# Performance work log

Measured on AMD Instinct MI355X. Metric: run time of the kernel, lower is better.

Reference implementation:

```python
import jax, jax.numpy as jnp
import numpy as np

B, S, D, H = 4, 2048, 1024, 16
DK = D // H

def setup_inputs() -> dict:
    key = jax.random.key(0)
    ks = jax.random.split(key, 7)
    f = lambda k, shape: jax.random.normal(k, shape, dtype=jnp.float32)
    return {
        "query": f(ks[0], (B, S, D)),
        "key":   f(ks[1], (B, S, D)),
        "value": f(ks[2], (B, S, D)),
        "w_q": f(ks[3], (D, D)) * (D ** -0.5),
        "w_k": f(ks[4], (D, D)) * (D ** -0.5),
        "w_v": f(ks[5], (D, D)) * (D ** -0.5),
        "w_o": f(ks[6], (D, D)) * (D ** -0.5),
    }

def reference(query, key, value, w_q, w_k, w_v, w_o):
    # Linear layers: y = x @ W^T (torch nn.Linear convention), bias=False
    def split_heads(x):  # [B,S,D] -> [B,H,S,DK]
        return x.reshape(B, S, H, DK).transpose(0, 2, 1, 3)
    Q = split_heads(query @ w_q.T)
    K = split_heads(key @ w_k.T)
    V = split_heads(value @ w_v.T)
    scale = jnp.float32(1.0 / np.sqrt(DK))
    scores = jnp.einsum('bhqd,bhkd->bhqk', Q, K) * scale  # [B,H,Sq,Sk]
    attn = jax.nn.softmax(scores, axis=-1)
    out = jnp.einsum('bhqk,bhkd->bhqd', attn, V)  # [B,H,Sq,DK]
    out = out.transpose(0, 2, 1, 3).reshape(B, S, D)
    return out @ w_o.T
```

## Files before the change

### kernel.cpp

```cpp
#include <hip/hip_runtime.h>
#include <stdint.h>

#define NB 4
#define NS 2048
#define ND 1024
#define NH 16
#define NDK 64
#define NM (NB*NS)

typedef __attribute__((ext_vector_type(8))) short short8;
typedef __attribute__((ext_vector_type(8))) unsigned short ushort8v;
typedef __attribute__((ext_vector_type(4))) float f32x4;
typedef __attribute__((ext_vector_type(16))) float f32x16;

__device__ __forceinline__ unsigned short f2bf(float f) {
  union { float f; uint32_t u; } v; v.f = f;
  uint32_t u = v.u;
  return (unsigned short)((u + 0x7FFFu + ((u >> 16) & 1u)) >> 16);
}

__device__ __forceinline__ void gload16(const void* g, void* l) {
  __builtin_amdgcn_global_load_lds(
      (const __attribute__((address_space(1))) void*)g,
      (__attribute__((address_space(3))) void*)l, 16, 0, 0);
}

__device__ __forceinline__ int xcd_swz(int flat, int nwg) {
  return (flat & 7) * (nwg >> 3) + (flat >> 3);
}

__global__ void convert_all(
    const float* __restrict__ x0, const float* __restrict__ x1, const float* __restrict__ x2,
    const float* __restrict__ w0, const float* __restrict__ w1,
    const float* __restrict__ w2, const float* __restrict__ w3,
    unsigned short* __restrict__ ox0, unsigned short* __restrict__ ox1, unsigned short* __restrict__ ox2,
    unsigned short* __restrict__ ow0, unsigned short* __restrict__ ow1,
    unsigned short* __restrict__ ow2, unsigned short* __restrict__ ow3)
{
  const float* src;
  unsigned short* dst;
  size_t i;
  if (blockIdx.y < 3) {
    src = blockIdx.y == 0 ? x0 : (blockIdx.y == 1 ? x1 : x2);
    dst = blockIdx.y == 0 ? ox0 : (blockIdx.y == 1 ? ox1 : ox2);
    i = ((size_t)blockIdx.x * 256 + threadIdx.x) * 8;
  } else {
    if (blockIdx.x >= 2048) return;
    size_t e = ((size_t)blockIdx.x * 256 + threadIdx.x) * 8;
    int which = (int)(e >> 20);
    size_t off = e & ((1u << 20) - 1);
    const float* ws[4] = {w0, w1, w2, w3};
    unsigned short* wd[4] = {ow0, ow1, ow2, ow3};
    src = ws[which]; dst = wd[which]; i = off;
  }
  f32x4 a = *(const f32x4*)(src + i);
  f32x4 b = *(const f32x4*)(src + i + 4);
  ushort8v h;
  h[0]=f2bf(a.x); h[1]=f2bf(a.y); h[2]=f2bf(a.z); h[3]=f2bf(a.w);
  h[4]=f2bf(b.x); h[5]=f2bf(b.y); h[6]=f2bf(b.z); h[7]=f2bf(b.w);
  *(ushort8v*)(dst + i) = h;
}

template<int OUT, int PRESCALE, int BN>
__device__ __forceinline__ void gemm_bk32_core(
    const unsigned short* __restrict__ A,
    const unsigned short* __restrict__ Bt,
    void* __restrict__ Cout,
    unsigned short* lds, int m0, int n0)
{
  const int K = ND, N = ND;
  const int NBF = BN / 64;
  const int NBL = BN / 128;
  const int NL  = 2 + NBL;
  const int ASZ = 8192, BSZ = BN*32, SZ = ASZ + BSZ;
  const int NT = K / 32;
  const int tid = threadIdx.x;
  const int lane = tid & 63, wid = tid >> 6;
  const int l15 = lane & 15, lg = lane >> 4;
  const int wr = wid >> 2, wc = wid & 3;
  const float QSC = 0.125f * 1.44269504088896f;

  const unsigned short* Asrc[2];
  const unsigned short* Bsrc[2];
  int dofA[2], dofB[2];
#pragma unroll
  for (int l = 0; l < 2; ++l) {
    int cidx = l*512 + tid;
    int r = cidx >> 2;
    int ch = (cidx & 3) ^ ((r >> 1) & 3);
    Asrc[l] = A + (size_t)(m0 + r)*K + ch*8;
    dofA[l] = cidx * 8;
  }
#pragma unroll
  for (int l = 0; l < NBL; ++l) {
    int cidx = l*512 + tid;
    int r = cidx >> 2;
    int ch = (cidx & 3) ^ ((r >> 1) & 3);
    Bsrc[l] = Bt + (size_t)(n0 + r)*K + ch*8;
    dofB[l] = cidx * 8;
  }

  f32x4 acc[8][NBF] = {};

#define STAGE32(t, buf)                                                        \
  {                                                                            \
    unsigned short* d_ = lds + (buf)*SZ;                                       \
    _Pragma("unroll") for (int l = 0; l < 2; ++l)                              \
      gload16(Asrc[l] + (t)*32, d_ + dofA[l]);                                 \
    _Pragma("unroll") for (int l = 0; l < NBL; ++l)                            \
      gload16(Bsrc[l] + (t)*32, d_ + ASZ + dofB[l]);                           \
  }

  STAGE32(0, 0)
  STAGE32(1, 1)
  if (NBL == 2) asm volatile("s_waitcnt vmcnt(4)" ::: "memory");
  else          asm volatile("s_waitcnt vmcnt(3)" ::: "memory");
  __builtin_amdgcn_s_barrier();

  int b0 = 0;
  for (int t = 0; t < NT; ++t) {
    if (t + 2 < NT) {
      int nb = b0 + 2; if (nb >= 3) nb -= 3;
      STAGE32(t + 2, nb)
    }
    const unsigned short* Abase = lds + b0*SZ;
    const unsigned short* Bbase = lds + b0*SZ + ASZ;

    short8 bfr[NBF];
#pragma unroll
    for (int nn = 0; nn < NBF; ++nn) {
      int row = wc*(BN/4) + nn*16 + l15;
      bfr[nn] = *(const short8*)(Bbase + row*32 + (lg ^ ((row >> 1) & 3))*8);
    }
#pragma unroll
    for (int mh = 0; mh < 2; ++mh) {
      short8 af[4];
#pragma unroll
      for (int mm = 0; mm < 4; ++mm) {
        int row = wr*128 + mh*64 + mm*16 + l15;
        af[mm] = *(const short8*)(Abase + row*32 + (lg ^ ((row >> 1) & 3))*8);
      }
      __builtin_amdgcn_s_setprio(1);
#pragma unroll
      for (int mm = 0; mm < 4; ++mm)
#pragma unroll
        for (int nn = 0; nn < NBF; ++nn)
          acc[mh*4+mm][nn] = __builtin_amdgcn_mfma_f32_16x16x32_bf16(
              af[mm], bfr[nn], acc[mh*4+mm][nn], 0, 0, 0);
      __builtin_amdgcn_s_setprio(0);
    }

    if (t + 2 < NT) {
      if (NBL == 2) asm volatile("s_waitcnt vmcnt(4)" ::: "memory");
      else          asm volatile("s_waitcnt vmcnt(3)" ::: "memory");
      __builtin_amdgcn_s_barrier();
    } else if (t + 1 < NT) {
      asm volatile("s_waitcnt vmcnt(0)" ::: "memory");
      __builtin_amdgcn_s_barrier();
    }
    b0 = (b0 + 1 == 3) ? 0 : b0 + 1;
  }
#undef STAGE32

#pragma unroll
  for (int m = 0; m < 8; ++m)
#pragma unroll
    for (int n = 0; n < NBF; ++n)
#pragma unroll
      for (int i = 0; i < 4; ++i) {
        int row = m0 + wr*128 + m*16 + lg*4 + i;
        int col = n0 + wc*(BN/4) + n*16 + l15;
        float val = PRESCALE ? acc[m][n][i] * QSC : acc[m][n][i];
        if (OUT == 0)
          ((float*)Cout)[(size_t)row * N + col] = val;
        else if (OUT == 1)
          ((unsigned short*)Cout)[(size_t)row * N + col] = f2bf(val);
        else
          ((unsigned short*)Cout)[((size_t)((row >> 11)*1024 + col))*NS + (row & (NS-1))]
              = f2bf(val);
      }
}

__global__ __launch_bounds__(512, 1) void gemm_qkv(
    const unsigned short* __restrict__ Xq, const unsigned short* __restrict__ Wq, unsigned short* Qb,
    const unsigned short* __restrict__ Xk, const unsigned short* __restrict__ Wk, unsigned short* Kb,
    const unsigned short* __restrict__ Xv, const unsigned short* __restrict__ Wv, unsigned short* VbT)
{
  __shared__ unsigned short lds[3*16384];
  int flat = (blockIdx.z * 32 + blockIdx.y) * 4 + blockIdx.x;
  int swz = xcd_swz(flat, 384);
  int z = swz >> 7, rem = swz & 127;
  int m0 = (rem >> 2) * 256, n0 = (rem & 3) * 256;
  if (z == 0)      gemm_bk32_core<1,1,256>(Xq, Wq, Qb,  lds, m0, n0);
  else if (z == 1) gemm_bk32_core<1,0,256>(Xk, Wk, Kb,  lds, m0, n0);
  else             gemm_bk32_core<2,0,256>(Xv, Wv, VbT, lds, m0, n0);
}

__global__ __launch_bounds__(512, 1) void gemm_o(
    const unsigned short* __restrict__ A, const unsigned short* __restrict__ Bt, float* C)
{
  __shared__ unsigned short lds[3*12288];
  int flat = blockIdx.y * 8 + blockIdx.x;
  int swz = xcd_swz(flat, 256);
  gemm_bk32_core<0,0,128>(A, Bt, C, lds, (swz >> 3) * 256, (swz & 7) * 128);
}

__global__ __launch_bounds__(256, 2) void flash_attn(
    const unsigned short* __restrict__ Qb,
    const unsigned short* __restrict__ Kb,
    const unsigned short* __restrict__ VT,
    unsigned short* __restrict__ O)
{
  __shared__ unsigned short Kt[2][64*64];
  __shared__ unsigned short Vt[2][64*64];
  const int tid = threadIdx.x, lane = tid & 63, wid = tid >> 6;
  const int l31 = lane & 31, hi = lane >> 5;
  int flat = blockIdx.y * 8 + blockIdx.x;
  int swz = xcd_swz(flat, 512);
  const int bh = swz >> 3, b = bh >> 4, h = bh & 15;
  const int q0 = (swz & 7) * 256 + wid * 64;

  const unsigned short* Kp[2]; const unsigned short* Vp[2]; int dofs[2];
#pragma unroll
  for (int p = 0; p < 2; ++p) {
    int slot = tid + p*256;
    int g = slot >> 6, r = slot & 63;
    Kp[p] = Kb + ((size_t)(b*NS + r))*ND + h*64 + g*8;
    Vp[p] = VT + ((size_t)(bh*64 + r))*NS + g*8;
    dofs[p] = slot * 8;
  }

  short8 qf[2][4];
#pragma unroll
  for (int qs = 0; qs < 2; ++qs)
#pragma unroll
    for (int ks = 0; ks < 4; ++ks)
      qf[qs][ks] = *(const short8*)(Qb + (size_t)(b*NS + q0 + qs*32 + l31)*ND + h*64 + ks*16 + hi*8);

  f32x16 oacc[2][2] = {};
  float lsum[2] = {0.f, 0.f};

#pragma unroll
  for (int p = 0; p < 2; ++p) {
    gload16(Kp[p], &Kt[0][dofs[p]]);
    gload16(Vp[p], &Vt[0][dofs[p]]);
  }
  __syncthreads();

  for (int t = 0; t < NS/64; ++t) {
    const int cur = t & 1;
    if (t + 1 < NS/64) {
#pragma unroll
      for (int p = 0; p < 2; ++p) {
        gload16(Kp[p] + (size_t)(t+1)*64*ND, &Kt[cur^1][dofs[p]]);
        gload16(Vp[p] + (t+1)*64,            &Vt[cur^1][dofs[p]]);
      }
    }
    const char* Kc = (const char*)Kt[cur];
    const char* Vc = (const char*)Vt[cur];

    short8 pa[2][2][2];
    float rs[2] = {0.f, 0.f};

#pragma unroll
    for (int n = 0; n < 2; ++n) {
      f32x16 st[2] = {};
      const int r = n*32 + l31;
      __builtin_amdgcn_s_setprio(1);
#pragma unroll
      for (int ks = 0; ks < 4; ++ks) {
        short8 kf = *(const short8*)(Kc + (((2*ks + hi) << 10) + r*16));
        st[0] = __builtin_amdgcn_mfma_f32_32x32x16_bf16(kf, qf[0][ks], st[0], 0, 0, 0);
        st[1] = __builtin_amdgcn_mfma_f32_32x32x16_bf16(kf, qf[1][ks], st[1], 0, 0, 0);
      }
      __builtin_amdgcn_s_setprio(0);
#pragma unroll
      for (int qs = 0; qs < 2; ++qs) {
        float lrs = 0.f;
#pragma unroll
        for (int e = 0; e < 16; ++e) {
          float p = __builtin_amdgcn_exp2f(st[qs][e]);
          st[qs][e] = p;
          lrs += p;
        }
        rs[qs] += lrs;
        uint32_t w[4][2];
#pragma unroll
        for (int e = 0; e < 4; ++e) {
          asm("v_cvt_pk_bf16_f32 %0, %1, %2"
              : "=v"(w[e][0]) : "v"(st[qs][4*e+0]), "v"(st[qs][4*e+1]));
          asm("v_cvt_pk_bf16_f32 %0, %1, %2"
              : "=v"(w[e][1]) : "v"(st[qs][4*e+2]), "v"(st[qs][4*e+3]));
        }
#pragma unroll
        for (int ksl = 0; ksl < 2; ++ksl) {
          uint32_t a0 = w[2*ksl][0], b0 = w[2*ksl+1][0];
          uint32_t a1 = w[2*ksl][1], b1 = w[2*ksl+1][1];
          asm("v_permlane32_swap_b32 %0, %1" : "+v"(a0), "+v"(b0));
          asm("v_permlane32_swap_b32 %0, %1" : "+v"(a1), "+v"(b1));
          union { uint32_t u[4]; short8 s; } f;
          f.u[0] = a0; f.u[1] = a1; f.u[2] = b0; f.u[3] = b1;
          pa[qs][n][ksl] = f.s;
        }
      }
    }
#pragma unroll
    for (int qs = 0; qs < 2; ++qs) {
      rs[qs] += __shfl_xor(rs[qs], 32);
      lsum[qs] += rs[qs];
    }

    __builtin_amdgcn_s_setprio(1);
#pragma unroll
    for (int d = 0; d < 2; ++d) {
      const int dr = d*32 + l31;
#pragma unroll
      for (int n = 0; n < 2; ++n)
#pragma unroll
        for (int ksl = 0; ksl < 2; ++ksl) {
          const int g = n*4 + ksl*2 + hi;
          short8 vf = *(const short8*)(Vc + ((g << 10) + dr*16));
          oacc[0][d] = __builtin_amdgcn_mfma_f32_32x32x16_bf16(pa[0][n][ksl], vf, oacc[0][d], 0, 0, 0);
          oacc[1][d] = __builtin_amdgcn_mfma_f32_32x32x16_bf16(pa[1][n][ksl], vf, oacc[1][d], 0, 0, 0);
        }
    }
    __builtin_amdgcn_s_setprio(0);
    __syncthreads();
  }

#pragma unroll
  for (int qs = 0; qs < 2; ++qs) {
    float linv[16];
#pragma unroll
    for (int r = 0; r < 16; ++r)
      linv[r] = 1.0f / __shfl(lsum[qs], (r & 3) + 8*(r >> 2) + 4*hi);
#pragma unroll
    for (int d = 0; d < 2; ++d)
#pragma unroll
      for (int r = 0; r < 16; ++r) {
        int qrow = q0 + qs*32 + (r & 3) + 8*(r >> 2) + 4*hi;
        O[(size_t)(b*NS + qrow)*ND + h*64 + d*32 + l31] = f2bf(oacc[qs][d][r] * linv[r]);
      }
  }
}

extern "C" void kernel_launch(void* const* d_in, const int* in_sizes, int n_in,
                              void* d_out, int out_size, void* d_ws, size_t ws_size,
                              hipStream_t stream) {
  const float* q  = (const float*)d_in[0];
  const float* k  = (const float*)d_in[1];
  const float* v  = (const float*)d_in[2];
  const float* wq = (const float*)d_in[3];
  const float* wk = (const float*)d_in[4];
  const float* wv = (const float*)d_in[5];
  const float* wo = (const float*)d_in[6];

  unsigned short* Wq = (unsigned short*)d_ws;
  unsigned short* Wk = Wq + (size_t)ND*ND;
  unsigned short* Wv = Wk + (size_t)ND*ND;
  unsigned short* Wo = Wv + (size_t)ND*ND;
  unsigned short* Xq = Wo + (size_t)ND*ND;
  unsigned short* Xk = Xq + (size_t)NM*ND;
  unsigned short* Xv = Xk + (size_t)NM*ND;
  unsigned short* Qb = Xv + (size_t)NM*ND;
  unsigned short* Kb = Qb + (size_t)NM*ND;
  unsigned short* VbT = (unsigned short*)d_out;
  unsigned short* Ob  = Xq;

  convert_all<<<dim3(NM*ND/(256*8), 4), 256, 0, stream>>>(
      q, k, v, wq, wk, wv, wo, Xq, Xk, Xv, Wq, Wk, Wv, Wo);

  gemm_qkv<<<dim3(4, 32, 3), 512, 0, stream>>>(Xq, Wq, Qb, Xk, Wk, Kb, Xv, Wv, VbT);

  flash_attn<<<dim3(8, 64), 256, 0, stream>>>(Qb, Kb, VbT, Ob);

  gemm_o<<<dim3(8, 32), 512, 0, stream>>>(Ob, Wo, (float*)d_out);
}
```

Baseline: 200.4 us.

## Fuse fp32-to-bf16 activation conversion into QKV GEMM and retile output GEMM

Drops the separate conversion pass for the three fp32 activation tensors. The QKV GEMM now stages raw fp32 A tiles into LDS with an XOR swizzle and converts them to bf16 in registers before the MFMA. This removes one full read and write of the bf16 activation copies, at the cost of twice the A-tile LDS and global traffic per stage and extra convert instructions in the inner loop. The output projection GEMM is rewritten as a standalone 128x128-tile kernel with more workgroups and two blocks per CU, to improve occupancy and load balance.

```diff
diff --git a/kernel.cpp b/kernel.cpp
--- a/kernel.cpp
+++ b/kernel.cpp
@@ -19,6 +19,12 @@
   return (unsigned short)((u + 0x7FFFu + ((u >> 16) & 1u)) >> 16);
 }
 
+__device__ __forceinline__ uint32_t cvtpk(float lo, float hi) {
+  uint32_t r;
+  asm("v_cvt_pk_bf16_f32 %0, %1, %2" : "=v"(r) : "v"(lo), "v"(hi));
+  return r;
+}
+
 __device__ __forceinline__ void gload16(const void* g, void* l) {
   __builtin_amdgcn_global_load_lds(
       (const __attribute__((address_space(1))) void*)g,
@@ -29,30 +35,19 @@
   return (flat & 7) * (nwg >> 3) + (flat >> 3);
 }
 
-__global__ void convert_all(
-    const float* __restrict__ x0, const float* __restrict__ x1, const float* __restrict__ x2,
+__global__ void convert_weights(
     const float* __restrict__ w0, const float* __restrict__ w1,
     const float* __restrict__ w2, const float* __restrict__ w3,
-    unsigned short* __restrict__ ox0, unsigned short* __restrict__ ox1, unsigned short* __restrict__ ox2,
     unsigned short* __restrict__ ow0, unsigned short* __restrict__ ow1,
     unsigned short* __restrict__ ow2, unsigned short* __restrict__ ow3)
 {
-  const float* src;
-  unsigned short* dst;
-  size_t i;
-  if (blockIdx.y < 3) {
-    src = blockIdx.y == 0 ? x0 : (blockIdx.y == 1 ? x1 : x2);
-    dst = blockIdx.y == 0 ? ox0 : (blockIdx.y == 1 ? ox1 : ox2);
-    i = ((size_t)blockIdx.x * 256 + threadIdx.x) * 8;
-  } else {
-    if (blockIdx.x >= 2048) return;
-    size_t e = ((size_t)blockIdx.x * 256 + threadIdx.x) * 8;
-    int which = (int)(e >> 20);
-    size_t off = e & ((1u << 20) - 1);
-    const float* ws[4] = {w0, w1, w2, w3};
-    unsigned short* wd[4] = {ow0, ow1, ow2, ow3};
-    src = ws[which]; dst = wd[which]; i = off;
-  }
+  size_t e = ((size_t)blockIdx.x * 256 + threadIdx.x) * 8;
+  int which = (int)(e >> 20);
+  size_t i = e & ((1u << 20) - 1);
+  const float* ws[4] = {w0, w1, w2, w3};
+  unsigned short* wd[4] = {ow0, ow1, ow2, ow3};
+  const float* src = ws[which];
+  unsigned short* dst = wd[which];
   f32x4 a = *(const f32x4*)(src + i);
   f32x4 b = *(const f32x4*)(src + i + 4);
   ushort8v h;
@@ -61,18 +56,15 @@
   *(ushort8v*)(dst + i) = h;
 }
 
-template<int OUT, int PRESCALE, int BN>
-__device__ __forceinline__ void gemm_bk32_core(
-    const unsigned short* __restrict__ A,
-    const unsigned short* __restrict__ Bt,
+template<int OUT, int PRESCALE>
+__device__ __forceinline__ void gemm_a32_core(
+    const float* __restrict__ X,
+    const unsigned short* __restrict__ Wt,
     void* __restrict__ Cout,
-    unsigned short* lds, int m0, int n0)
+    char* lds, int m0, int n0)
 {
   const int K = ND, N = ND;
-  const int NBF = BN / 64;
-  const int NBL = BN / 128;
-  const int NL  = 2 + NBL;
-  const int ASZ = 8192, BSZ = BN*32, SZ = ASZ + BSZ;
+  const int SZB = 49152;
   const int NT = K / 32;
   const int tid = threadIdx.x;
   const int lane = tid & 63, wid = tid >> 6;
@@ -80,57 +72,57 @@
   const int wr = wid >> 2, wc = wid & 3;
   const float QSC = 0.125f * 1.44269504088896f;
 
-  const unsigned short* Asrc[2];
+  const float* Asrc[4];
+  int dofA[4];
+#pragma unroll
+  for (int l = 0; l < 4; ++l) {
+    int cidx = l*512 + tid;
+    int r = cidx >> 3;
+    int c = (cidx & 7) ^ (r & 7);
+    Asrc[l] = X + (size_t)(m0 + r)*K + c*4;
+    dofA[l] = cidx * 16;
+  }
   const unsigned short* Bsrc[2];
-  int dofA[2], dofB[2];
+  int dofB[2];
 #pragma unroll
   for (int l = 0; l < 2; ++l) {
     int cidx = l*512 + tid;
     int r = cidx >> 2;
-    int ch = (cidx & 3) ^ ((r >> 1) & 3);
-    Asrc[l] = A + (size_t)(m0 + r)*K + ch*8;
-    dofA[l] = cidx * 8;
-  }
-#pragma unroll
-  for (int l = 0; l < NBL; ++l) {
-    int cidx = l*512 + tid;
-    int r = cidx >> 2;
-    int ch = (cidx & 3) ^ ((r >> 1) & 3);
-    Bsrc[l] = Bt + (size_t)(n0 + r)*K + ch*8;
-    dofB[l] = cidx * 8;
-  }
-
-  f32x4 acc[8][NBF] = {};
-
-#define STAGE32(t, buf)                                                        \
+    int c = (cidx & 3) ^ ((r >> 1) & 3);
+    Bsrc[l] = Wt + (size_t)(n0 + r)*K + c*8;
+    dofB[l] = cidx * 16;
+  }
+
+  f32x4 acc[8][4] = {};
+
+#define STAGEQ(t, buf)                                                         \
   {                                                                            \
-    unsigned short* d_ = lds + (buf)*SZ;                                       \
+    char* d_ = lds + (buf)*SZB;                                                \
+    _Pragma("unroll") for (int l = 0; l < 4; ++l)                              \
+      gload16(Asrc[l] + (t)*32, d_ + dofA[l]);                                 \
     _Pragma("unroll") for (int l = 0; l < 2; ++l)                              \
-      gload16(Asrc[l] + (t)*32, d_ + dofA[l]);                                 \
-    _Pragma("unroll") for (int l = 0; l < NBL; ++l)                            \
-      gload16(Bsrc[l] + (t)*32, d_ + ASZ + dofB[l]);                           \
-  }
-
-  STAGE32(0, 0)
-  STAGE32(1, 1)
-  if (NBL == 2) asm volatile("s_waitcnt vmcnt(4)" ::: "memory");
-  else          asm volatile("s_waitcnt vmcnt(3)" ::: "memory");
+      gload16(Bsrc[l] + (t)*32, d_ + 32768 + dofB[l]);                         \
+  }
+
+  STAGEQ(0, 0)
+  STAGEQ(1, 1)
+  asm volatile("s_waitcnt vmcnt(6)" ::: "memory");
   __builtin_amdgcn_s_barrier();
 
   int b0 = 0;
   for (int t = 0; t < NT; ++t) {
     if (t + 2 < NT) {
       int nb = b0 + 2; if (nb >= 3) nb -= 3;
-      STAGE32(t + 2, nb)
-    }
-    const unsigned short* Abase = lds + b0*SZ;
-    const unsigned short* Bbase = lds + b0*SZ + ASZ;
-
-    short8 bfr[NBF];
-#pragma unroll
-    for (int nn = 0; nn < NBF; ++nn) {
-      int row = wc*(BN/4) + nn*16 + l15;
-      bfr[nn] = *(const short8*)(Bbase + row*32 + (lg ^ ((row >> 1) & 3))*8);
+      STAGEQ(t + 2, nb)
+    }
+    const char* Ab = lds + b0*SZB;
+    const unsigned short* Bb = (const unsigned short*)(lds + b0*SZB + 32768);
+
+    short8 bfr[4];
+#pragma unroll
+    for (int nn = 0; nn < 4; ++nn) {
+      int row = wc*64 + nn*16 + l15;
+      bfr[nn] = *(const short8*)(Bb + row*32 + (lg ^ ((row >> 1) & 3))*8);
     }
 #pragma unroll
     for (int mh = 0; mh < 2; ++mh) {
@@ -138,21 +130,27 @@
 #pragma unroll
       for (int mm = 0; mm < 4; ++mm) {
         int row = wr*128 + mh*64 + mm*16 + l15;
-        af[mm] = *(const short8*)(Abase + row*32 + (lg ^ ((row >> 1) & 3))*8);
+        const char* Ar = Ab + row*128;
+        int c0 = (2*lg) ^ (row & 7), c1 = (2*lg + 1) ^ (row & 7);
+        f32x4 a0 = *(const f32x4*)(Ar + c0*16);
+        f32x4 a1 = *(const f32x4*)(Ar + c1*16);
+        union { uint32_t u[4]; short8 s; } f;
+        f.u[0] = cvtpk(a0.x, a0.y); f.u[1] = cvtpk(a0.z, a0.w);
+        f.u[2] = cvtpk(a1.x, a1.y); f.u[3] = cvtpk(a1.z, a1.w);
+        af[mm] = f.s;
       }
       __builtin_amdgcn_s_setprio(1);
 #pragma unroll
       for (int mm = 0; mm < 4; ++mm)
 #pragma unroll
-        for (int nn = 0; nn < NBF; ++nn)
+        for (int nn = 0; nn < 4; ++nn)
           acc[mh*4+mm][nn] = __builtin_amdgcn_mfma_f32_16x16x32_bf16(
               af[mm], bfr[nn], acc[mh*4+mm][nn], 0, 0, 0);
       __builtin_amdgcn_s_setprio(0);
     }
 
     if (t + 2 < NT) {
-      if (NBL == 2) asm volatile("s_waitcnt vmcnt(4)" ::: "memory");
-      else          asm volatile("s_waitcnt vmcnt(3)" ::: "memory");
+      asm volatile("s_waitcnt vmcnt(6)" ::: "memory");
       __builtin_amdgcn_s_barrier();
     } else if (t + 1 < NT) {
       asm volatile("s_waitcnt vmcnt(0)" ::: "memory");
@@ -160,20 +158,18 @@
     }
     b0 = (b0 + 1 == 3) ? 0 : b0 + 1;
   }
-#undef STAGE32
+#undef STAGEQ
 
 #pragma unroll
   for (int m = 0; m < 8; ++m)
 #pragma unroll
-    for (int n = 0; n < NBF; ++n)
+    for (int n = 0; n < 4; ++n)
 #pragma unroll
       for (int i = 0; i < 4; ++i) {
         int row = m0 + wr*128 + m*16 + lg*4 + i;
-        int col = n0 + wc*(BN/4) + n*16 + l15;
+        int col = n0 + wc*64 + n*16 + l15;
         float val = PRESCALE ? acc[m][n][i] * QSC : acc[m][n][i];
-        if (OUT == 0)
-          ((float*)Cout)[(size_t)row * N + col] = val;
-        else if (OUT == 1)
+        if (OUT == 1)
           ((unsigned short*)Cout)[(size_t)row * N + col] = f2bf(val);
         else
           ((unsigned short*)Cout)[((size_t)((row >> 11)*1024 + col))*NS + (row & (NS-1))]
@@ -182,27 +178,112 @@
 }
 
 __global__ __launch_bounds__(512, 1) void gemm_qkv(
-    const unsigned short* __restrict__ Xq, const unsigned short* __restrict__ Wq, unsigned short* Qb,
-    const unsigned short* __restrict__ Xk, const unsigned short* __restrict__ Wk, unsigned short* Kb,
-    const unsigned short* __restrict__ Xv, const unsigned short* __restrict__ Wv, unsigned short* VbT)
+    const float* __restrict__ Xq, const unsigned short* __restrict__ Wq, unsigned short* Qb,
+    const float* __restrict__ Xk, const unsigned short* __restrict__ Wk, unsigned short* Kb,
+    const float* __restrict__ Xv, const unsigned short* __restrict__ Wv, unsigned short* VbT)
 {
-  __shared__ unsigned short lds[3*16384];
+  __shared__ char lds[3*49152];
   int flat = (blockIdx.z * 32 + blockIdx.y) * 4 + blockIdx.x;
   int swz = xcd_swz(flat, 384);
   int z = swz >> 7, rem = swz & 127;
   int m0 = (rem >> 2) * 256, n0 = (rem & 3) * 256;
-  if (z == 0)      gemm_bk32_core<1,1,256>(Xq, Wq, Qb,  lds, m0, n0);
-  else if (z == 1) gemm_bk32_core<1,0,256>(Xk, Wk, Kb,  lds, m0, n0);
-  else             gemm_bk32_core<2,0,256>(Xv, Wv, VbT, lds, m0, n0);
-}
-
-__global__ __launch_bounds__(512, 1) void gemm_o(
+  if (z == 0)      gemm_a32_core<1,1>(Xq, Wq, Qb,  lds, m0, n0);
+  else if (z == 1) gemm_a32_core<1,0>(Xk, Wk, Kb,  lds, m0, n0);
+  else             gemm_a32_core<2,0>(Xv, Wv, VbT, lds, m0, n0);
+}
+
+__global__ __launch_bounds__(512, 2) void gemm_o(
     const unsigned short* __restrict__ A, const unsigned short* __restrict__ Bt, float* C)
 {
-  __shared__ unsigned short lds[3*12288];
+  __shared__ unsigned short lds[3*8192];
+  const int K = ND, N = ND;
+  const int SZ = 8192;
+  const int NT = K / 32;
+  const int tid = threadIdx.x;
+  const int lane = tid & 63, wid = tid >> 6;
+  const int l15 = lane & 15, lg = lane >> 4;
+  const int wr = wid >> 2, wc = wid & 3;
   int flat = blockIdx.y * 8 + blockIdx.x;
-  int swz = xcd_swz(flat, 256);
-  gemm_bk32_core<0,0,128>(A, Bt, C, lds, (swz >> 3) * 256, (swz & 7) * 128);
+  int swz = xcd_swz(flat, 512);
+  const int m0 = (swz >> 3) * 128, n0 = (swz & 7) * 128;
+
+  const unsigned short* Asrc;
+  const unsigned short* Bsrc;
+  int dofA, dofB;
+  {
+    int r = tid >> 2;
+    int c = (tid & 3) ^ ((r >> 1) & 3);
+    Asrc = A  + (size_t)(m0 + r)*K + c*8;
+    Bsrc = Bt + (size_t)(n0 + r)*K + c*8;
+    dofA = tid * 8;
+    dofB = 4096 + tid * 8;
+  }
+
+  f32x4 acc[4][2] = {};
+
+#define STAGEO(t, buf)                                                         \
+  {                                                                            \
+    unsigned short* d_ = lds + (buf)*SZ;                                       \
+    gload16(Asrc + (t)*32, d_ + dofA);                                         \
+    gload16(Bsrc + (t)*32, d_ + dofB);                                         \
+  }
+
+  STAGEO(0, 0)
+  STAGEO(1, 1)
+  asm volatile("s_waitcnt vmcnt(2)" ::: "memory");
+  __builtin_amdgcn_s_barrier();
+
+  int b0 = 0;
+  for (int t = 0; t < NT; ++t) {
+    if (t + 2 < NT) {
+      int nb = b0 + 2; if (nb >= 3) nb -= 3;
+      STAGEO(t + 2, nb)
+    }
+    const unsigned short* Abase = lds + b0*SZ;
+    const unsigned short* Bbase = lds + b0*SZ + 4096;
+
+    short8 bfr[2];
+#pragma unroll
+    for (int nn = 0; nn < 2; ++nn) {
+      int row = wc*32 + nn*16 + l15;
+      bfr[nn] = *(const short8*)(Bbase + row*32 + (lg ^ ((row >> 1) & 3))*8);
+    }
+    short8 af[4];
+#pragma unroll
+    for (int mm = 0; mm < 4; ++mm) {
+      int row = wr*64 + mm*16 + l15;
+      af[mm] = *(const short8*)(Abase + row*32 + (lg ^ ((row >> 1) & 3))*8);
+    }
+    __builtin_amdgcn_s_setprio(1);
+#pragma unroll
+    for (int mm = 0; mm < 4; ++mm)
+#pragma unroll
+      for (int nn = 0; nn < 2; ++nn)
+        acc[mm][nn] = __builtin_amdgcn_mfma_f32_16x16x32_bf16(
+            af[mm], bfr[nn], acc[mm][nn], 0, 0, 0);
+    __builtin_amdgcn_s_setprio(0);
+
+    if (t + 2 < NT) {
+      asm volatile("s_waitcnt vmcnt(2)" ::: "memory");
+      __builtin_amdgcn_s_barrier();
+    } else if (t + 1 < NT) {
+      asm volatile("s_waitcnt vmcnt(0)" ::: "memory");
+      __builtin_amdgcn_s_barrier();
+    }
+    b0 = (b0 + 1 == 3) ? 0 : b0 + 1;
+  }
+#undef STAGEO
+
+#pragma unroll
+  for (int m = 0; m < 4; ++m)
+#pragma unroll
+    for (int n = 0; n < 2; ++n)
+#pragma unroll
+      for (int i = 0; i < 4; ++i) {
+        int row = m0 + wr*64 + m*16 + lg*4 + i;
+        int col = n0 + wc*32 + n*16 + l15;
+        C[(size_t)row * N + col] = acc[m][n][i];
+      }
 }
 
 __global__ __launch_bounds__(256, 2) void flash_attn(
@@ -287,10 +368,8 @@
         uint32_t w[4][2];
 #pragma unroll
         for (int e = 0; e < 4; ++e) {
-          asm("v_cvt_pk_bf16_f32 %0, %1, %2"
-              : "=v"(w[e][0]) : "v"(st[qs][4*e+0]), "v"(st[qs][4*e+1]));
-          asm("v_cvt_pk_bf16_f32 %0, %1, %2"
-              : "=v"(w[e][1]) : "v"(st[qs][4*e+2]), "v"(st[qs][4*e+3]));
+          w[e][0] = cvtpk(st[qs][4*e+0], st[qs][4*e+1]);
+          w[e][1] = cvtpk(st[qs][4*e+2], st[qs][4*e+3]);
         }
 #pragma unroll
         for (int ksl = 0; ksl < 2; ++ksl) {
@@ -359,20 +438,16 @@
   unsigned short* Wk = Wq + (size_t)ND*ND;
   unsigned short* Wv = Wk + (size_t)ND*ND;
   unsigned short* Wo = Wv + (size_t)ND*ND;
-  unsigned short* Xq = Wo + (size_t)ND*ND;
-  unsigned short* Xk = Xq + (size_t)NM*ND;
-  unsigned short* Xv = Xk + (size_t)NM*ND;
-  unsigned short* Qb = Xv + (size_t)NM*ND;
+  unsigned short* Qb = Wo + (size_t)ND*ND;
   unsigned short* Kb = Qb + (size_t)NM*ND;
+  unsigned short* Ob = Kb + (size_t)NM*ND;
   unsigned short* VbT = (unsigned short*)d_out;
-  unsigned short* Ob  = Xq;
-
-  convert_all<<<dim3(NM*ND/(256*8), 4), 256, 0, stream>>>(
-      q, k, v, wq, wk, wv, wo, Xq, Xk, Xv, Wq, Wk, Wv, Wo);
-
-  gemm_qkv<<<dim3(4, 32, 3), 512, 0, stream>>>(Xq, Wq, Qb, Xk, Wk, Kb, Xv, Wv, VbT);
+
+  convert_weights<<<2048, 256, 0, stream>>>(wq, wk, wv, wo, Wq, Wk, Wv, Wo);
+
+  gemm_qkv<<<dim3(4, 32, 3), 512, 0, stream>>>(q, Wq, Qb, k, Wk, Kb, v, Wv, VbT);
 
   flash_attn<<<dim3(8, 64), 256, 0, stream>>>(Qb, Kb, VbT, Ob);
 
-  gemm_o<<<dim3(8, 32), 512, 0, stream>>>(Ob, Wo, (float*)d_out);
-}
+  gemm_o<<<dim3(8, 64), 512, 0, stream>>>(Ob, Wo, (float*)d_out);
+}
```

After: 200.1 us. No clear change (-0.1%).
